# Kernel tuning notes

Measured on AMD Instinct MI355X. Metric: run time of the kernel, lower is better.

## Reference

```python
import jax, jax.numpy as jnp
import numpy as np

EPS = 1e-8            # EpisodicMemory.eps
TEMPERATURE = 0.25    # default temperature in query()


def setup_inputs() -> dict:
    key = jax.random.key(0)
    k1, k2, k3 = jax.random.split(key, 3)
    B, N, KD, VD, TOPK = 512, 500000, 128, 64, 16
    queries = jax.random.normal(k1, (B, KD), dtype=jnp.float32)
    # stored keys are L2-normalized at insert time
    keys = jax.random.normal(k2, (N, KD), dtype=jnp.float32)
    keys = keys / jnp.clip(jnp.linalg.norm(keys, axis=1, keepdims=True), EPS, None)
    values = jax.random.normal(k3, (N, VD), dtype=jnp.float32)
    return {"queries": queries, "keys": keys, "values": values, "topk": TOPK}


def reference(queries, keys, values, topk):
    # cosine similarity: normalize queries (keys already normalized in memory)
    qn = queries / jnp.clip(jnp.linalg.norm(queries, axis=1, keepdims=True), EPS, None)
    scores = (qn @ keys.T) / max(1e-6, TEMPERATURE)          # [B, N]
    topv, topidx = jax.lax.top_k(scores, topk)               # [B, K], [B, K]
    # stable exp-softmax with eps in the denominator (as in torch source)
    topv_exp = jnp.exp(topv - jnp.max(topv, axis=1, keepdims=True))
    topw = topv_exp / (jnp.sum(topv_exp, axis=1, keepdims=True) + EPS)
    vals = values[topidx]                                    # gather: [B, K, VD]
    retrieved = jnp.einsum('bk,bkd->bd', topw, vals)         # [B, VD]
    return retrieved, topw, topidx
```

## Files before the change

kernel.cpp:

```cpp
#include <hip/hip_runtime.h>
#include <hip/hip_bf16.h>

#define NB 512
#define KD 128
#define VD 64
#define NKEYS 500000
#define TOPK 16
#define CH 1024
#define NCHUNK 489
#define CPC 8
#define NCAND (NCHUNK*CPC)
#define CBUF 64
#define JCAND 16

typedef __attribute__((ext_vector_type(8))) short bf8s;
typedef __attribute__((ext_vector_type(4))) float f4;
typedef __attribute__((ext_vector_type(4))) int i4;

__device__ __forceinline__ unsigned f2bf(float x) {
  union { float f; unsigned u; } v; v.f = x;
  return (v.u + 0x7fffu + ((v.u >> 16) & 1u)) >> 16;
}

__global__ __launch_bounds__(128) void qnorm_kernel(const float* __restrict__ q,
                                                    float* __restrict__ qn_f,
                                                    short* __restrict__ qn_bf) {
  int b = blockIdx.x, t = threadIdx.x;
  float x = q[b*KD + t];
  float s = x * x;
  #pragma unroll
  for (int o = 32; o > 0; o >>= 1) s += __shfl_down(s, o);
  __shared__ float p[2];
  if ((t & 63) == 0) p[t >> 6] = s;
  __syncthreads();
  float norm = sqrtf(p[0] + p[1]);
  norm = fmaxf(norm, 1e-8f);
  float v = x * (4.0f / norm);
  qn_f[b*KD + t] = v;
  qn_bf[b*KD + t] = (short)f2bf(v);
}

__global__ __launch_bounds__(256) void score_filter_kernel(
    const float* __restrict__ keys, const short* __restrict__ qn_bf,
    float* __restrict__ cand_val, int* __restrict__ cand_idx) {
  __shared__ float slds[4*64*17];
  const int bid = blockIdx.x;
  const int chunk = (bid & 7) + 8*(bid >> 6);
  const int gy    = (bid >> 3) & 7;
  if (chunk >= NCHUNK) return;
  const int tid  = threadIdx.x;
  const int wave = tid >> 6, lane = tid & 63;
  const int col  = lane & 15, quad = lane >> 4;

  bf8s afrag[4][4];
  const int qbase = gy*64;
  #pragma unroll
  for (int mt = 0; mt < 4; mt++)
    #pragma unroll
    for (int ks = 0; ks < 4; ks++)
      afrag[mt][ks] = *(const bf8s*)(qn_bf + (qbase + mt*16 + col)*KD + ks*32 + quad*8);

  float tv0=-1e30f, tv1=-1e30f, tv2=-1e30f, tv3=-1e30f;
  int   ti0=0, ti1=0, ti2=0, ti3=0;
  const int k0 = chunk*CH + wave*256;

  f4 x0[4], x1[4];
  {
    int r = k0 + col; if (r > NKEYS-1) r = NKEYS-1;
    const float* kp = keys + (size_t)r*KD + quad*8;
    #pragma unroll
    for (int ks = 0; ks < 4; ks++) {
      x0[ks] = *(const f4*)(kp + ks*32);
      x1[ks] = *(const f4*)(kp + ks*32 + 4);
    }
  }

  #pragma unroll 1
  for (int t16 = 0; t16 < 16; t16++) {
    const int nb = k0 + t16*16;
    bf8s bfrag[4];
    #pragma unroll
    for (int ks = 0; ks < 4; ks++) {
      bf8s tt;
      tt[0]=(short)f2bf(x0[ks][0]); tt[1]=(short)f2bf(x0[ks][1]);
      tt[2]=(short)f2bf(x0[ks][2]); tt[3]=(short)f2bf(x0[ks][3]);
      tt[4]=(short)f2bf(x1[ks][0]); tt[5]=(short)f2bf(x1[ks][1]);
      tt[6]=(short)f2bf(x1[ks][2]); tt[7]=(short)f2bf(x1[ks][3]);
      bfrag[ks] = tt;
    }
    if (t16 < 15) {
      int r = nb + 16 + col; if (r > NKEYS-1) r = NKEYS-1;
      const float* kp = keys + (size_t)r*KD + quad*8;
      #pragma unroll
      for (int ks = 0; ks < 4; ks++) {
        x0[ks] = *(const f4*)(kp + ks*32);
        x1[ks] = *(const f4*)(kp + ks*32 + 4);
      }
    }
    f4 acc[4];
    #pragma unroll
    for (int mt = 0; mt < 4; mt++) { acc[mt][0]=0.f; acc[mt][1]=0.f; acc[mt][2]=0.f; acc[mt][3]=0.f; }
    #pragma unroll
    for (int ks = 0; ks < 4; ks++)
      #pragma unroll
      for (int mt = 0; mt < 4; mt++)
        acc[mt] = __builtin_amdgcn_mfma_f32_16x16x32_bf16(afrag[mt][ks], bfrag[ks], acc[mt], 0, 0, 0);
    #pragma unroll
    for (int mt = 0; mt < 4; mt++)
      #pragma unroll
      for (int rg = 0; rg < 4; rg++)
        slds[wave*1088 + (mt*16 + quad*4 + rg)*17 + col] = acc[mt][rg];
    #pragma unroll
    for (int c = 0; c < 16; c++) {
      int n = nb + c;
      float v = slds[wave*1088 + lane*17 + c];
      if (v > tv3 && n < NKEYS) {
        if (v > tv0)      { tv3=tv2;ti3=ti2; tv2=tv1;ti2=ti1; tv1=tv0;ti1=ti0; tv0=v;ti0=n; }
        else if (v > tv1) { tv3=tv2;ti3=ti2; tv2=tv1;ti2=ti1; tv1=v;ti1=n; }
        else if (v > tv2) { tv3=tv2;ti3=ti2; tv2=v;ti2=n; }
        else              { tv3=v;ti3=n; }
      }
    }
  }

  __syncthreads();
  float* fv = slds;
  int*   fi = (int*)(slds + 1024);
  const int pb = wave*256 + lane*4;
  fv[pb+0]=tv0; fv[pb+1]=tv1; fv[pb+2]=tv2; fv[pb+3]=tv3;
  fi[pb+0]=ti0; fi[pb+1]=ti1; fi[pb+2]=ti2; fi[pb+3]=ti3;
  __syncthreads();
  if (tid < 64) {
    float bv[8]; int bi[8];
    #pragma unroll
    for (int k = 0; k < 8; k++) { bv[k] = -1e30f; bi[k] = 0; }
    #pragma unroll
    for (int w = 0; w < 4; w++)
      #pragma unroll
      for (int j = 0; j < 4; j++) {
        float v = fv[w*256 + tid*4 + j];
        int  ix = fi[w*256 + tid*4 + j];
        if (v > bv[7]) {
          bv[7] = v; bi[7] = ix;
          #pragma unroll
          for (int s = 7; s > 0; s--)
            if (bv[s] > bv[s-1]) {
              float tv = bv[s]; bv[s] = bv[s-1]; bv[s-1] = tv;
              int   ti = bi[s]; bi[s] = bi[s-1]; bi[s-1] = ti;
            }
        }
      }
    const size_t o = ((size_t)(qbase + tid)*NCHUNK + chunk)*CPC;
    f4 v0; v0[0]=bv[0]; v0[1]=bv[1]; v0[2]=bv[2]; v0[3]=bv[3];
    f4 v1; v1[0]=bv[4]; v1[1]=bv[5]; v1[2]=bv[6]; v1[3]=bv[7];
    i4 j0; j0[0]=bi[0]; j0[1]=bi[1]; j0[2]=bi[2]; j0[3]=bi[3];
    i4 j1; j1[0]=bi[4]; j1[1]=bi[5]; j1[2]=bi[6]; j1[3]=bi[7];
    *(f4*)(cand_val + o)     = v0;
    *(f4*)(cand_val + o + 4) = v1;
    *(i4*)(cand_idx + o)     = j0;
    *(i4*)(cand_idx + o + 4) = j1;
  }
}

__global__ __launch_bounds__(256) void merge_rescore_kernel(
    const float* __restrict__ qn_f, const float* __restrict__ keys,
    const float* __restrict__ values, const float* __restrict__ cand_val,
    const int* __restrict__ cand_idx, float* __restrict__ out) {
  const int b = blockIdx.x, t = threadIdx.x;
  const int lane = t & 63, wave = t >> 6;
  __shared__ float qs[KD];
  __shared__ unsigned hist[256];
  __shared__ int wtot[4];
  __shared__ int s_bound, s_above, s_bcnt, s_cnt;
  __shared__ float rv[CBUF]; __shared__ int ri[CBUF];
  __shared__ float sval[TOPK]; __shared__ int sidx[TOPK]; __shared__ float sw[TOPK];

  if (t < KD) qs[t] = qn_f[b*KD + t];

  unsigned u[JCAND]; int id[JCAND];
  #pragma unroll
  for (int j = 0; j < JCAND; j++) {
    int i = t + j*256;
    if (i < NCAND) {
      union { float f; unsigned q; } cvt; cvt.f = cand_val[(size_t)b*NCAND + i];
      unsigned m = cvt.q;
      m = (m & 0x80000000u) ? ~m : (m | 0x80000000u);
      u[j] = m; id[j] = cand_idx[(size_t)b*NCAND + i];
    } else { u[j] = 0u; id[j] = -1; }
  }

  unsigned prefix = 0; int above = 0; unsigned thr = 0; bool done = false;
  #pragma unroll 1
  for (int pass = 0; pass < 3 && !done; pass++) {
    const int shift = 24 - 8*pass;
    hist[t] = 0u;
    __syncthreads();
    #pragma unroll
    for (int j = 0; j < JCAND; j++) {
      bool ok = (pass == 0) || ((u[j] >> (shift + 8)) == prefix);
      if (ok) atomicAdd(&hist[(u[j] >> shift) & 255u], 1u);
    }
    __syncthreads();
    int h = (int)hist[t];
    int s = h;
    #pragma unroll
    for (int o = 1; o < 64; o <<= 1) {
      int nv = __shfl_down(s, o);
      if (lane + o < 64) s += nv;
    }
    if (lane == 0) wtot[wave] = s;
    __syncthreads();
    int add = 0;
    for (int g = wave + 1; g < 4; g++) add += wtot[g];
    int S = s + add;
    if (above + S >= 32 && above + S - h < 32) {
      s_bound = t; s_above = above + S - h; s_bcnt = h;
    }
    __syncthreads();
    prefix = (prefix << 8) | (unsigned)s_bound;
    above  = s_above;
    if (s_above + s_bcnt <= CBUF || pass == 2) { thr = prefix << shift; done = true; }
    __syncthreads();
  }

  if (t == 0) s_cnt = 0;
  __syncthreads();
  #pragma unroll
  for (int j = 0; j < JCAND; j++) {
    if (id[j] >= 0 && u[j] >= thr) {
      int p = atomicAdd(&s_cnt, 1);
      if (p < CBUF) ri[p] = id[j];
    }
  }
  __syncthreads();
  const int C = min(s_cnt, CBUF);
  if (t >= C && t < CBUF) ri[t] = 0x7fffffff;
  __syncthreads();

  {
    int c = t >> 2, dg = t & 3;
    float part = 0.f;
    if (c < C) {
      const float* kr = keys + (size_t)ri[c]*KD + dg*32;
      #pragma unroll
      for (int j = 0; j < 32; j++) part += kr[j] * qs[dg*32 + j];
    }
    part += __shfl_down(part, 2, 4);
    part += __shfl_down(part, 1, 4);
    if (dg == 0) rv[c] = (c < C) ? part : -1e30f;
  }
  __syncthreads();

  if (t < CBUF) {
    float v = rv[t]; int idx = ri[t];
    int rank = 0;
    for (int j = 0; j < CBUF; j++) {
      float vj = rv[j]; int ij = ri[j];
      rank += (vj > v) || (vj == v && ij < idx);
    }
    if (rank < TOPK) { sval[rank] = v; sidx[rank] = idx; }
  }
  __syncthreads();

  if (t < TOPK) {
    float m = sval[0];
    float e = expf(sval[t] - m);
    float s2 = e;
    #pragma unroll
    for (int o = 8; o > 0; o >>= 1) s2 += __shfl_down(s2, o, 16);
    s2 = __shfl(s2, 0, 16);
    float w = e / (s2 + 1e-8f);
    sw[t] = w;
    out[NB*VD + b*TOPK + t] = w;
    out[NB*VD + NB*TOPK + b*TOPK + t] = (float)sidx[t];
  }
  __syncthreads();

  if (t < VD) {
    float acc = 0.f;
    #pragma unroll
    for (int k = 0; k < TOPK; k++) acc += sw[k] * values[(size_t)sidx[k]*VD + t];
    out[b*VD + t] = acc;
  }
}

extern "C" void kernel_launch(void* const* d_in, const int* in_sizes, int n_in,
                              void* d_out, int out_size, void* d_ws, size_t ws_size,
                              hipStream_t stream) {
  const float* queries = (const float*)d_in[0];
  const float* keys    = (const float*)d_in[1];
  const float* values  = (const float*)d_in[2];
  float* out = (float*)d_out;

  char* ws = (char*)d_ws;
  float* qn_f  = (float*)ws;
  short* qn_bf = (short*)(ws + (size_t)NB*KD*4);
  float* cand_val = (float*)(ws + (size_t)NB*KD*4 + (size_t)NB*KD*2);
  int*   cand_idx = (int*)((char*)cand_val + (size_t)NB*NCAND*sizeof(float));

  qnorm_kernel<<<NB, KD, 0, stream>>>(queries, qn_f, qn_bf);
  score_filter_kernel<<<62*64, 256, 0, stream>>>(keys, qn_bf, cand_val, cand_idx);
  merge_rescore_kernel<<<NB, 256, 0, stream>>>(qn_f, keys, values, cand_val, cand_idx, out);
}
```

Baseline: 628.9 us.

## Pre-convert keys to bf16 and pack candidate indices into score low bits

```diff
diff --git a/kernel.cpp b/kernel.cpp
--- a/kernel.cpp
+++ b/kernel.cpp
@@ -8,6 +8,7 @@
 #define TOPK 16
 #define CH 1024
 #define NCHUNK 489
+#define NKEYSP (NCHUNK*CH)
 #define CPC 8
 #define NCAND (NCHUNK*CPC)
 #define CBUF 64
@@ -16,6 +17,7 @@
 typedef __attribute__((ext_vector_type(8))) short bf8s;
 typedef __attribute__((ext_vector_type(4))) float f4;
 typedef __attribute__((ext_vector_type(4))) int i4;
+typedef __attribute__((ext_vector_type(4))) unsigned u4;
 
 __device__ __forceinline__ unsigned f2bf(float x) {
   union { float f; unsigned u; } v; v.f = x;
@@ -40,10 +42,25 @@
   qn_bf[b*KD + t] = (short)f2bf(v);
 }
 
+__global__ __launch_bounds__(256) void kconv_kernel(const float* __restrict__ keys,
+                                                    unsigned short* __restrict__ kbf) {
+  size_t i = ((size_t)blockIdx.x*256 + threadIdx.x)*8;
+  f4 a = *(const f4*)(keys + i);
+  f4 b = *(const f4*)(keys + i + 4);
+  u4 p;
+  p[0] = f2bf(a[0]) | (f2bf(a[1]) << 16);
+  p[1] = f2bf(a[2]) | (f2bf(a[3]) << 16);
+  p[2] = f2bf(b[0]) | (f2bf(b[1]) << 16);
+  p[3] = f2bf(b[2]) | (f2bf(b[3]) << 16);
+  *(u4*)(kbf + i) = p;
+}
+
+template<int MODE>
 __global__ __launch_bounds__(256) void score_filter_kernel(
-    const float* __restrict__ keys, const short* __restrict__ qn_bf,
+    const float* __restrict__ keysf, const unsigned short* __restrict__ keysb,
+    const short* __restrict__ qn_bf,
     float* __restrict__ cand_val, int* __restrict__ cand_idx) {
-  __shared__ float slds[4*64*17];
+  __shared__ float slds[4*64*20];
   const int bid = blockIdx.x;
   const int chunk = (bid & 7) + 8*(bid >> 6);
   const int gy    = (bid >> 3) & 7;
@@ -61,85 +78,119 @@
       afrag[mt][ks] = *(const bf8s*)(qn_bf + (qbase + mt*16 + col)*KD + ks*32 + quad*8);
 
   float tv0=-1e30f, tv1=-1e30f, tv2=-1e30f, tv3=-1e30f;
-  int   ti0=0, ti1=0, ti2=0, ti3=0;
   const int k0 = chunk*CH + wave*256;
-
-  f4 x0[4], x1[4];
-  {
-    int r = k0 + col; if (r > NKEYS-1) r = NKEYS-1;
-    const float* kp = keys + (size_t)r*KD + quad*8;
+  const bool tailw = (k0 + 256 > NKEYS);
+
+  float* wp = slds + wave*1280;
+  const float* sp = wp + lane*20;
+
+  bf8s bfA[4], bfB[4];
+  f4   xbA[8], xbB[8];
+
+  if constexpr (MODE == 0) {
+    const unsigned short* kp = keysb + (size_t)(k0 + col)*KD + quad*8;
+    #pragma unroll
+    for (int ks = 0; ks < 4; ks++) bfA[ks] = *(const bf8s*)(kp + ks*32);
+  } else {
+    int r = min(k0 + col, NKEYS-1);
+    const float* kp = keysf + (size_t)r*KD + quad*8;
     #pragma unroll
     for (int ks = 0; ks < 4; ks++) {
-      x0[ks] = *(const f4*)(kp + ks*32);
-      x1[ks] = *(const f4*)(kp + ks*32 + 4);
-    }
-  }
+      xbA[2*ks]   = *(const f4*)(kp + ks*32);
+      xbA[2*ks+1] = *(const f4*)(kp + ks*32 + 4);
+    }
+  }
+
+  auto tile_body = [&](int t16, bf8s (&bfC)[4], bf8s (&bfN)[4],
+                       f4 (&xbC)[8], f4 (&xbN)[8]) {
+    const int nb16 = k0 + t16*16;
+    if (t16 < 15) {
+      if constexpr (MODE == 0) {
+        const unsigned short* kp = keysb + (size_t)(nb16 + 16 + col)*KD + quad*8;
+        #pragma unroll
+        for (int ks = 0; ks < 4; ks++) bfN[ks] = *(const bf8s*)(kp + ks*32);
+      } else {
+        int r = min(nb16 + 16 + col, NKEYS-1);
+        const float* kp = keysf + (size_t)r*KD + quad*8;
+        #pragma unroll
+        for (int ks = 0; ks < 4; ks++) {
+          xbN[2*ks]   = *(const f4*)(kp + ks*32);
+          xbN[2*ks+1] = *(const f4*)(kp + ks*32 + 4);
+        }
+      }
+    }
+    bf8s bcur[4];
+    if constexpr (MODE == 0) {
+      #pragma unroll
+      for (int ks = 0; ks < 4; ks++) bcur[ks] = bfC[ks];
+    } else {
+      #pragma unroll
+      for (int ks = 0; ks < 4; ks++) {
+        union { unsigned u[4]; bf8s b; } t;
+        f4 a = xbC[2*ks], b = xbC[2*ks+1];
+        t.u[0] = f2bf(a[0]) | (f2bf(a[1]) << 16);
+        t.u[1] = f2bf(a[2]) | (f2bf(a[3]) << 16);
+        t.u[2] = f2bf(b[0]) | (f2bf(b[1]) << 16);
+        t.u[3] = f2bf(b[2]) | (f2bf(b[3]) << 16);
+        bcur[ks] = t.b;
+      }
+    }
+    f4 acc[4];
+    #pragma unroll
+    for (int mt = 0; mt < 4; mt++) { acc[mt][0]=0.f; acc[mt][1]=0.f; acc[mt][2]=0.f; acc[mt][3]=0.f; }
+    #pragma unroll
+    for (int ks = 0; ks < 4; ks++)
+      #pragma unroll
+      for (int mt = 0; mt < 4; mt++)
+        acc[mt] = __builtin_amdgcn_mfma_f32_16x16x32_bf16(afrag[mt][ks], bcur[ks], acc[mt], 0, 0, 0);
+    const unsigned kbase = (unsigned)(t16*16 + col);
+    #pragma unroll
+    for (int mt = 0; mt < 4; mt++)
+      #pragma unroll
+      for (int rg = 0; rg < 4; rg++) {
+        float v = acc[mt][rg];
+        if (tailw) v = (nb16 + col < NKEYS) ? v : -1e30f;
+        unsigned pv = (__float_as_uint(v) & 0xFFFFFF00u) | kbase;
+        wp[(mt*16 + quad*4 + rg)*20 + col] = __uint_as_float(pv);
+      }
+    #pragma unroll
+    for (int j = 0; j < 4; j++) {
+      f4 g = *(const f4*)(sp + j*4);
+      #pragma unroll
+      for (int c = 0; c < 4; c++) {
+        float v = g[c];
+        if (v > tv3) {
+          if (v > tv0)      { tv3=tv2; tv2=tv1; tv1=tv0; tv0=v; }
+          else if (v > tv1) { tv3=tv2; tv2=tv1; tv1=v; }
+          else if (v > tv2) { tv3=tv2; tv2=v; }
+          else              { tv3=v; }
+        }
+      }
+    }
+  };
 
   #pragma unroll 1
-  for (int t16 = 0; t16 < 16; t16++) {
-    const int nb = k0 + t16*16;
-    bf8s bfrag[4];
-    #pragma unroll
-    for (int ks = 0; ks < 4; ks++) {
-      bf8s tt;
-      tt[0]=(short)f2bf(x0[ks][0]); tt[1]=(short)f2bf(x0[ks][1]);
-      tt[2]=(short)f2bf(x0[ks][2]); tt[3]=(short)f2bf(x0[ks][3]);
-      tt[4]=(short)f2bf(x1[ks][0]); tt[5]=(short)f2bf(x1[ks][1]);
-      tt[6]=(short)f2bf(x1[ks][2]); tt[7]=(short)f2bf(x1[ks][3]);
-      bfrag[ks] = tt;
-    }
-    if (t16 < 15) {
-      int r = nb + 16 + col; if (r > NKEYS-1) r = NKEYS-1;
-      const float* kp = keys + (size_t)r*KD + quad*8;
-      #pragma unroll
-      for (int ks = 0; ks < 4; ks++) {
-        x0[ks] = *(const f4*)(kp + ks*32);
-        x1[ks] = *(const f4*)(kp + ks*32 + 4);
-      }
-    }
-    f4 acc[4];
-    #pragma unroll
-    for (int mt = 0; mt < 4; mt++) { acc[mt][0]=0.f; acc[mt][1]=0.f; acc[mt][2]=0.f; acc[mt][3]=0.f; }
-    #pragma unroll
-    for (int ks = 0; ks < 4; ks++)
-      #pragma unroll
-      for (int mt = 0; mt < 4; mt++)
-        acc[mt] = __builtin_amdgcn_mfma_f32_16x16x32_bf16(afrag[mt][ks], bfrag[ks], acc[mt], 0, 0, 0);
-    #pragma unroll
-    for (int mt = 0; mt < 4; mt++)
-      #pragma unroll
-      for (int rg = 0; rg < 4; rg++)
-        slds[wave*1088 + (mt*16 + quad*4 + rg)*17 + col] = acc[mt][rg];
-    #pragma unroll
-    for (int c = 0; c < 16; c++) {
-      int n = nb + c;
-      float v = slds[wave*1088 + lane*17 + c];
-      if (v > tv3 && n < NKEYS) {
-        if (v > tv0)      { tv3=tv2;ti3=ti2; tv2=tv1;ti2=ti1; tv1=tv0;ti1=ti0; tv0=v;ti0=n; }
-        else if (v > tv1) { tv3=tv2;ti3=ti2; tv2=tv1;ti2=ti1; tv1=v;ti1=n; }
-        else if (v > tv2) { tv3=tv2;ti3=ti2; tv2=v;ti2=n; }
-        else              { tv3=v;ti3=n; }
-      }
-    }
+  for (int t2 = 0; t2 < 8; t2++) {
+    tile_body(2*t2,     bfA, bfB, xbA, xbB);
+    tile_body(2*t2 + 1, bfB, bfA, xbB, xbA);
   }
 
   __syncthreads();
   float* fv = slds;
-  int*   fi = (int*)(slds + 1024);
   const int pb = wave*256 + lane*4;
   fv[pb+0]=tv0; fv[pb+1]=tv1; fv[pb+2]=tv2; fv[pb+3]=tv3;
-  fi[pb+0]=ti0; fi[pb+1]=ti1; fi[pb+2]=ti2; fi[pb+3]=ti3;
   __syncthreads();
   if (tid < 64) {
     float bv[8]; int bi[8];
     #pragma unroll
     for (int k = 0; k < 8; k++) { bv[k] = -1e30f; bi[k] = 0; }
     #pragma unroll
-    for (int w = 0; w < 4; w++)
+    for (int w = 0; w < 4; w++) {
+      const int kw = chunk*CH + w*256;
       #pragma unroll
       for (int j = 0; j < 4; j++) {
         float v = fv[w*256 + tid*4 + j];
-        int  ix = fi[w*256 + tid*4 + j];
+        int  ix = kw + (int)(__float_as_uint(v) & 0xFFu);
         if (v > bv[7]) {
           bv[7] = v; bi[7] = ix;
           #pragma unroll
@@ -150,6 +201,7 @@
             }
         }
       }
+    }
     const size_t o = ((size_t)(qbase + tid)*NCHUNK + chunk)*CPC;
     f4 v0; v0[0]=bv[0]; v0[1]=bv[1]; v0[2]=bv[2]; v0[3]=bv[3];
     f4 v1; v1[0]=bv[4]; v1[1]=bv[5]; v1[2]=bv[6]; v1[3]=bv[7];
@@ -297,8 +349,17 @@
   short* qn_bf = (short*)(ws + (size_t)NB*KD*4);
   float* cand_val = (float*)(ws + (size_t)NB*KD*4 + (size_t)NB*KD*2);
   int*   cand_idx = (int*)((char*)cand_val + (size_t)NB*NCAND*sizeof(float));
+  unsigned short* kbf = (unsigned short*)((char*)cand_idx + (size_t)NB*NCAND*sizeof(int));
+
+  const size_t need = (size_t)NB*KD*4 + (size_t)NB*KD*2
+                    + (size_t)NB*NCAND*8 + (size_t)NKEYSP*KD*2;
 
   qnorm_kernel<<<NB, KD, 0, stream>>>(queries, qn_f, qn_bf);
-  score_filter_kernel<<<62*64, 256, 0, stream>>>(keys, qn_bf, cand_val, cand_idx);
+  if (ws_size >= need) {
+    kconv_kernel<<<(NKEYS*KD)/(256*8), 256, 0, stream>>>(keys, kbf);
+    score_filter_kernel<0><<<62*64, 256, 0, stream>>>(keys, kbf, qn_bf, cand_val, cand_idx);
+  } else {
+    score_filter_kernel<1><<<62*64, 256, 0, stream>>>(keys, nullptr, qn_bf, cand_val, cand_idx);
+  }
   merge_rescore_kernel<<<NB, 256, 0, stream>>>(qn_f, keys, values, cand_val, cand_idx, out);
 }
```

New measurement: 1.323 ms. 110% more time.
